# Optimization experiments

Hardware: AMD Instinct MI355X
Metric: run time of the kernel (lower is better)

## Reference

```python
import jax, jax.numpy as jnp
import numpy as np

N = 500000   # total objects across all segments
B = 8192     # number of segments (batch)
OBJ = 64     # object_size
H = 128      # hidden_size
CTX = 256    # context_size


def setup_inputs() -> dict:
    key = jax.random.key(0)
    ks = jax.random.split(key, 9)
    s = 0.05
    x = jax.random.normal(ks[0], (N, OBJ), jnp.float32)
    context = jax.random.normal(ks[1], (B, CTX), jnp.float32)
    # sorted segment ids, every segment nonempty (ragged lengths collapse to ~N/B each)
    segment_ids = (jnp.arange(N, dtype=jnp.int32) * B) // N
    W0 = jax.random.normal(ks[2], (OBJ, H), jnp.float32) * s
    b0 = jnp.zeros((H,), jnp.float32)
    W1 = jax.random.normal(ks[3], (H, H), jnp.float32) * s
    b1 = jnp.zeros((H,), jnp.float32)
    Wkv = jax.random.normal(ks[4], (H, 2 * H), jnp.float32) * s
    bkv = jnp.zeros((2 * H,), jnp.float32)
    Wq = jax.random.normal(ks[5], (CTX, H), jnp.float32) * s
    bq = jnp.zeros((H,), jnp.float32)
    gain = jnp.full((1, 1), -0.5 * np.log(H), jnp.float32)
    return dict(x=x, context=context, segment_ids=segment_ids,
                W0=W0, b0=b0, W1=W1, b1=b1, Wkv=Wkv, bkv=bkv,
                Wq=Wq, bq=bq, gain=gain)


def reference(x, context, segment_ids, W0, b0, W1, b1, Wkv, bkv, Wq, bq, gain):
    h = jax.nn.relu(x @ W0 + b0)          # [N, H]
    h = jax.nn.relu(h @ W1 + b1)          # [N, H]
    kv = h @ Wkv + bkv                    # [N, 2H]
    hsz = Wkv.shape[1] // 2
    key_, value = kv[:, :hsz], kv[:, hsz:]
    q = context @ Wq + bq                 # [B, H]
    qg = q[segment_ids]                   # gather == repeat_interleave
    logits = jnp.exp(gain)[0, 0] * jnp.sum(key_ * qg, axis=1)  # [N]
    # per-segment stable softmax
    m = jax.ops.segment_max(logits, segment_ids, num_segments=B)
    z = jnp.exp(logits - m[segment_ids])
    denom = jax.ops.segment_sum(z, segment_ids, num_segments=B)
    w = z / denom[segment_ids]            # [N]
    # per-segment softmax-weighted sum of values -> [B, H]
    embedding = jax.ops.segment_sum(w[:, None] * value, segment_ids, num_segments=B)
    return embedding, w[:, None]
```

## Files before the change

### kernel.cpp

```cpp
#include <hip/hip_runtime.h>
#include <math.h>

#define NN   500000
#define BB   8192
#define OBJ  64
#define HH   128
#define CTXD 256

typedef __attribute__((ext_vector_type(8))) short short8;
typedef __attribute__((ext_vector_type(4))) float f32x4;

#define W0HI  0
#define W0LO  8192
#define W1HI  16384
#define W1LO  32768
#define QG_OFF  98304
#define PG_OFF  4292608
#define CQ_OFF  8486912
#define WS_NEED 8519680

__device__ __forceinline__ unsigned short f2bf(float f) {
    unsigned int u = __float_as_uint(f);
    u += 0x7FFFu + ((u >> 16) & 1u);
    return (unsigned short)(u >> 16);
}
__device__ __forceinline__ float bf2f(unsigned short h) {
    return __uint_as_float(((unsigned int)h) << 16);
}
__device__ __forceinline__ void split2(float v, unsigned short& hi, unsigned short& lo) {
    unsigned int u = __float_as_uint(v);
    hi = (unsigned short)(u >> 16);
    lo = f2bf(v - bf2f(hi));
}

__global__ void prep_frags(const float* __restrict__ W0,
                           const float* __restrict__ W1,
                           unsigned short* __restrict__ wsb)
{
    const int t = blockIdx.x * 256 + threadIdx.x;
    if (t >= 48 * 64) return;
    const int f = t >> 6, lane = t & 63;
    const float* W; int KS, bhi, blo, fl;
    if (f < 16) { W = W0; KS = 2; bhi = W0HI; blo = W0LO; fl = f; }
    else        { W = W1; KS = 4; bhi = W1HI; blo = W1LO; fl = f - 16; }
    const int nt = fl / KS, ks = fl - nt * KS;
    const int n  = nt * 16 + (lane & 15);
    const int k0 = ks * 32 + (lane >> 4) * 8;
    short8 h8, l8;
    #pragma unroll
    for (int j = 0; j < 8; ++j) {
        float v = W[(size_t)(k0 + j) * HH + n];
        unsigned short h, l; split2(v, h, l);
        h8[j] = (short)h; l8[j] = (short)l;
    }
    const int off = fl * 512 + lane * 8;
    *(short8*)(wsb + bhi + off) = h8;
    *(short8*)(wsb + blo + off) = l8;
}

__global__ void q_gemm(const float* __restrict__ context,
                       const float* __restrict__ Wq,
                       const float* __restrict__ bq,
                       float* __restrict__ qg)
{
    __shared__ float ctxs[16 * CTXD];
    const int tid = threadIdx.x;
    const int seg0 = blockIdx.x * 16;
    {
        const float4* cg = (const float4*)(context + (size_t)seg0 * CTXD);
        float4* cs = (float4*)ctxs;
        for (int i = tid; i < 16 * CTXD / 4; i += 128) cs[i] = cg[i];
    }
    __syncthreads();
    float acc[16];
    const float bqv = bq[tid];
    #pragma unroll
    for (int s = 0; s < 16; ++s) acc[s] = bqv;
    #pragma unroll 4
    for (int k = 0; k < CTXD; ++k) {
        const float wv = Wq[(size_t)k * HH + tid];
        #pragma unroll
        for (int s = 0; s < 16; ++s) acc[s] = fmaf(ctxs[s * CTXD + k], wv, acc[s]);
    }
    #pragma unroll
    for (int s = 0; s < 16; ++s) qg[(size_t)(seg0 + s) * HH + tid] = acc[s];
}

__global__ void p_gemm(const float* __restrict__ qg,
                       const float* __restrict__ Wkv,
                       const float* __restrict__ bkv,
                       float* __restrict__ pg, float* __restrict__ cq)
{
    __shared__ float qs[16 * HH];
    const int tid = threadIdx.x;
    const int seg0 = blockIdx.x * 16;
    {
        const float4* sg = (const float4*)(qg + (size_t)seg0 * HH);
        float4* ss = (float4*)qs;
        for (int i = tid; i < 16 * HH / 4; i += 128) ss[i] = sg[i];
    }
    __syncthreads();
    float acc[16];
    #pragma unroll
    for (int s = 0; s < 16; ++s) acc[s] = 0.f;
    for (int c = 0; c < HH; ++c) {
        const float wv = Wkv[(size_t)tid * 2 * HH + c];
        #pragma unroll
        for (int s = 0; s < 16; ++s) acc[s] = fmaf(qs[s * HH + c], wv, acc[s]);
    }
    #pragma unroll
    for (int s = 0; s < 16; ++s) pg[(size_t)(seg0 + s) * HH + tid] = acc[s];
    if (tid < 16) {
        float a = 0.f;
        for (int c = 0; c < HH; ++c) a = fmaf(bkv[c], qs[tid * HH + c], a);
        cq[seg0 + tid] = a;
    }
}

#define BS 40

__launch_bounds__(64, 1)
__global__ void seg_wave(const float* __restrict__ x,
                         const float* __restrict__ context,
                         const float* __restrict__ Wq,   const float* __restrict__ bq,
                         const float* __restrict__ Wkv,  const float* __restrict__ bkv,
                         const float* __restrict__ b0,
                         const float* __restrict__ b1,
                         const float* __restrict__ gain,
                         const unsigned short* __restrict__ wsb,
                         const float* __restrict__ pg,
                         const float* __restrict__ cq,
                         float* __restrict__ out_emb, float* __restrict__ out_w)
{
    __shared__ unsigned short smem[2 * 64 * BS];
    const int lane = threadIdx.x;
    const int seg  = blockIdx.x;
    const int nl = lane & 15, q = lane >> 4;

    unsigned short* bufh = smem;
    unsigned short* bufl = smem + 64 * BS;
    float* fscr = (float*)smem;

    const int start = (int)(((long long)seg * NN + BB - 1) / BB);
    const int end   = (int)(((long long)(seg + 1) * NN + BB - 1) / BB);
    const int count = end - start;

    float b0v[8], b1v[8];
    #pragma unroll
    for (int nt = 0; nt < 8; ++nt) { b0v[nt] = b0[nt * 16 + nl]; b1v[nt] = b1[nt * 16 + nl]; }

    short8 axh[2][4], axl[2][4];
    #pragma unroll
    for (int ks = 0; ks < 2; ++ks) {
        #pragma unroll
        for (int mt = 0; mt < 4; ++mt) {
            int row = start + mt * 16 + nl;
            if (row > NN - 1) row = NN - 1;
            const float* xp = x + (size_t)row * OBJ + ks * 32 + q * 8;
            const float4 a0 = *(const float4*)xp;
            const float4 a1 = *(const float4*)(xp + 4);
            const float vv[8] = {a0.x, a0.y, a0.z, a0.w, a1.x, a1.y, a1.z, a1.w};
            #pragma unroll
            for (int j = 0; j < 8; ++j) {
                unsigned short h, l; split2(vv[j], h, l);
                axh[ks][mt][j] = (short)h; axl[ks][mt][j] = (short)l;
            }
        }
    }

    f32x4 acc2[8][4];
    #pragma unroll
    for (int nt = 0; nt < 8; ++nt)
        #pragma unroll
        for (int mt = 0; mt < 4; ++mt) acc2[nt][mt] = {0.f, 0.f, 0.f, 0.f};

    #pragma unroll
    for (int j = 0; j < 4; ++j) {
        f32x4 a1acc[2][4];
        #pragma unroll
        for (int t = 0; t < 2; ++t)
            #pragma unroll
            for (int mt = 0; mt < 4; ++mt) a1acc[t][mt] = {0.f, 0.f, 0.f, 0.f};
        #pragma unroll
        for (int ks = 0; ks < 2; ++ks) {
            #pragma unroll
            for (int t = 0; t < 2; ++t) {
                const int fb = ((2 * j + t) * 2 + ks) * 512 + lane * 8;
                const short8 bh = *(const short8*)(wsb + W0HI + fb);
                const short8 bl = *(const short8*)(wsb + W0LO + fb);
                #pragma unroll
                for (int mt = 0; mt < 4; ++mt) {
                    a1acc[t][mt] = __builtin_amdgcn_mfma_f32_16x16x32_bf16(axh[ks][mt], bh, a1acc[t][mt], 0, 0, 0);
                    a1acc[t][mt] = __builtin_amdgcn_mfma_f32_16x16x32_bf16(axh[ks][mt], bl, a1acc[t][mt], 0, 0, 0);
                    a1acc[t][mt] = __builtin_amdgcn_mfma_f32_16x16x32_bf16(axl[ks][mt], bh, a1acc[t][mt], 0, 0, 0);
                }
            }
        }
        #pragma unroll
        for (int t = 0; t < 2; ++t) {
            const float bb = b0v[2 * j + t];
            #pragma unroll
            for (int mt = 0; mt < 4; ++mt) {
                #pragma unroll
                for (int r = 0; r < 4; ++r) {
                    const int R = mt * 16 + q * 4 + r;
                    float hv = fmaxf(a1acc[t][mt][r] + bb, 0.f);
                    unsigned short h, l; split2(hv, h, l);
                    bufh[R * BS + t * 16 + nl] = h;
                    bufl[R * BS + t * 16 + nl] = l;
                }
            }
        }
        __asm__ volatile("s_waitcnt lgkmcnt(0)" ::: "memory");
        short8 ah[4], al[4];
        #pragma unroll
        for (int mt = 0; mt < 4; ++mt) {
            ah[mt] = *(const short8*)(bufh + (mt * 16 + nl) * BS + q * 8);
            al[mt] = *(const short8*)(bufl + (mt * 16 + nl) * BS + q * 8);
        }
        #pragma unroll
        for (int nt = 0; nt < 8; ++nt) {
            const int fb = (nt * 4 + j) * 512 + lane * 8;
            const short8 bh = *(const short8*)(wsb + W1HI + fb);
            const short8 bl = *(const short8*)(wsb + W1LO + fb);
            #pragma unroll
            for (int mt = 0; mt < 4; ++mt) {
                acc2[nt][mt] = __builtin_amdgcn_mfma_f32_16x16x32_bf16(ah[mt], bh, acc2[nt][mt], 0, 0, 0);
                acc2[nt][mt] = __builtin_amdgcn_mfma_f32_16x16x32_bf16(ah[mt], bl, acc2[nt][mt], 0, 0, 0);
                acc2[nt][mt] = __builtin_amdgcn_mfma_f32_16x16x32_bf16(al[mt], bh, acc2[nt][mt], 0, 0, 0);
            }
        }
        __asm__ volatile("s_waitcnt lgkmcnt(0)" ::: "memory");
    }

    #pragma unroll
    for (int nt = 0; nt < 8; ++nt)
        #pragma unroll
        for (int mt = 0; mt < 4; ++mt)
            #pragma unroll
            for (int r = 0; r < 4; ++r)
                acc2[nt][mt][r] = fmaxf(acc2[nt][mt][r] + b1v[nt], 0.f);

    float pv[8], cqv;
    if (pg) {
        #pragma unroll
        for (int nt = 0; nt < 8; ++nt) pv[nt] = pg[(size_t)seg * HH + nt * 16 + nl];
        cqv = cq[seg];
    } else {
        const int c0 = lane, c1 = lane + 64;
        float qa = bq[c0], qb = bq[c1];
        for (int k = 0; k < CTXD; ++k) {
            const float ck = context[(size_t)seg * CTXD + k];
            qa = fmaf(ck, Wq[(size_t)k * HH + c0], qa);
            qb = fmaf(ck, Wq[(size_t)k * HH + c1], qb);
        }
        fscr[c0] = qa; fscr[c1] = qb;
        __asm__ volatile("s_waitcnt lgkmcnt(0)" ::: "memory");
        cqv = 0.f;
        for (int c = 0; c < HH; ++c) cqv = fmaf(bkv[c], fscr[c], cqv);
        #pragma unroll
        for (int nt = 0; nt < 8; ++nt) {
            const int k = nt * 16 + nl;
            float s = 0.f;
            for (int c = 0; c < HH; ++c) s = fmaf(Wkv[(size_t)k * 2 * HH + c], fscr[c], s);
            pv[nt] = s;
        }
        __asm__ volatile("s_waitcnt lgkmcnt(0)" ::: "memory");
    }

    const float eg = expf(gain[0]);
    float lp[4][4];
    #pragma unroll
    for (int mt = 0; mt < 4; ++mt) {
        #pragma unroll
        for (int r = 0; r < 4; ++r) {
            float s = 0.f;
            #pragma unroll
            for (int nt = 0; nt < 8; ++nt) s = fmaf(acc2[nt][mt][r], pv[nt], s);
            #pragma unroll
            for (int off = 1; off <= 8; off <<= 1) s += __shfl_xor(s, off, 64);
            const int row = mt * 16 + q * 4 + r;
            lp[mt][r] = (row < count) ? eg * (s + cqv) : -INFINITY;
        }
    }

    float m = lp[0][0];
    #pragma unroll
    for (int mt = 0; mt < 4; ++mt)
        #pragma unroll
        for (int r = 0; r < 4; ++r) m = fmaxf(m, lp[mt][r]);
    m = fmaxf(m, __shfl_xor(m, 16, 64));
    m = fmaxf(m, __shfl_xor(m, 32, 64));
    float wv[4][4], Z = 0.f;
    #pragma unroll
    for (int mt = 0; mt < 4; ++mt)
        #pragma unroll
        for (int r = 0; r < 4; ++r) { wv[mt][r] = expf(lp[mt][r] - m); Z += wv[mt][r]; }
    Z += __shfl_xor(Z, 16, 64);
    Z += __shfl_xor(Z, 32, 64);
    const float rZ = 1.f / Z;
    #pragma unroll
    for (int mt = 0; mt < 4; ++mt)
        #pragma unroll
        for (int r = 0; r < 4; ++r) wv[mt][r] *= rZ;
    if (nl == 0) {
        #pragma unroll
        for (int mt = 0; mt < 4; ++mt)
            #pragma unroll
            for (int r = 0; r < 4; ++r) {
                const int row = mt * 16 + q * 4 + r;
                if (row < count) out_w[start + row] = wv[mt][r];
            }
    }

    float un[8];
    #pragma unroll
    for (int nt = 0; nt < 8; ++nt) {
        float s = 0.f;
        #pragma unroll
        for (int mt = 0; mt < 4; ++mt)
            #pragma unroll
            for (int r = 0; r < 4; ++r) s = fmaf(wv[mt][r], acc2[nt][mt][r], s);
        s += __shfl_xor(s, 16, 64);
        s += __shfl_xor(s, 32, 64);
        un[nt] = s;
    }
    __asm__ volatile("s_waitcnt lgkmcnt(0)" ::: "memory");
    if (q == 0) {
        #pragma unroll
        for (int nt = 0; nt < 8; ++nt) fscr[nt * 16 + nl] = un[nt];
    }
    __asm__ volatile("s_waitcnt lgkmcnt(0)" ::: "memory");

    {
        const int c0 = lane, c1 = lane + 64;
        float e0 = bkv[HH + c0], e1 = bkv[HH + c1];
        #pragma unroll 4
        for (int k = 0; k < HH; ++k) {
            const float uk = fscr[k];
            e0 = fmaf(uk, Wkv[(size_t)k * 2 * HH + HH + c0], e0);
            e1 = fmaf(uk, Wkv[(size_t)k * 2 * HH + HH + c1], e1);
        }
        out_emb[(size_t)seg * HH + c0] = e0;
        out_emb[(size_t)seg * HH + c1] = e1;
    }
}

extern "C" void kernel_launch(void* const* d_in, const int* in_sizes, int n_in,
                              void* d_out, int out_size, void* d_ws, size_t ws_size,
                              hipStream_t stream)
{
    (void)in_sizes; (void)n_in; (void)out_size;
    const float* x    = (const float*)d_in[0];
    const float* ctx  = (const float*)d_in[1];
    const float* W0   = (const float*)d_in[3];
    const float* b0   = (const float*)d_in[4];
    const float* W1   = (const float*)d_in[5];
    const float* b1   = (const float*)d_in[6];
    const float* Wkv  = (const float*)d_in[7];
    const float* bkv  = (const float*)d_in[8];
    const float* Wq   = (const float*)d_in[9];
    const float* bq   = (const float*)d_in[10];
    const float* gain = (const float*)d_in[11];

    float* out_emb = (float*)d_out;
    float* out_w   = (float*)d_out + (size_t)BB * HH;

    unsigned short* wsb = (unsigned short*)d_ws;
    const bool big_ws = (ws_size >= (size_t)WS_NEED);
    float* qg = big_ws ? (float*)((char*)d_ws + QG_OFF) : nullptr;
    float* pg = big_ws ? (float*)((char*)d_ws + PG_OFF) : nullptr;
    float* cq = big_ws ? (float*)((char*)d_ws + CQ_OFF) : nullptr;

    hipLaunchKernelGGL(prep_frags, dim3(12), dim3(256), 0, stream, W0, W1, wsb);
    if (big_ws) {
        hipLaunchKernelGGL(q_gemm, dim3(BB / 16), dim3(128), 0, stream, ctx, Wq, bq, qg);
        hipLaunchKernelGGL(p_gemm, dim3(BB / 16), dim3(128), 0, stream, qg, Wkv, bkv, pg, cq);
    }
    hipLaunchKernelGGL(seg_wave, dim3(BB), dim3(64), 0, stream,
                       x, ctx, Wq, bq, Wkv, bkv, b0, b1, gain, wsb, pg, cq,
                       out_emb, out_w);
}
```

Baseline: 413.6 us.

## Stage x tiles in swizzled LDS, split embedding GEMM out, transpose Wkv for p_gemm

The x tile is now converted to bf16 hi/lo pairs into XOR-swizzled shared memory instead of being held as register fragments. Hidden activations also move to a swizzled layout, and launch bounds rise to two waves per SIMD to improve occupancy. The final value projection leaves the per-segment wave: unnormalised sums go to a workspace buffer and a separate batched emb_gemm kernel applies Wkv. p_gemm reads a pre-transposed Wkv for coalesced loads. In exchange, the change adds two kernel launches and more global traffic, and it depends on the workspace overlap of qg and ug being safe.

```diff
diff --git a/kernel.cpp b/kernel.cpp
--- a/kernel.cpp
+++ b/kernel.cpp
@@ -14,10 +14,12 @@
 #define W0LO  8192
 #define W1HI  16384
 #define W1LO  32768
-#define QG_OFF  98304
-#define PG_OFF  4292608
-#define CQ_OFF  8486912
-#define WS_NEED 8519680
+#define WKT_OFF 98304
+#define QG_OFF  163840
+#define UG_OFF  163840
+#define PG_OFF  4358144
+#define CQ_OFF  8552448
+#define WS_NEED 8585216
 
 __device__ __forceinline__ unsigned short f2bf(float f) {
     unsigned int u = __float_as_uint(f);
@@ -58,6 +60,16 @@
     *(short8*)(wsb + blo + off) = l8;
 }
 
+__global__ void wk_t(const float* __restrict__ Wkv, float* __restrict__ wkt)
+{
+    __shared__ float tile[16][17];
+    const int tx = threadIdx.x, ty = threadIdx.y;
+    const int k0 = blockIdx.x * 16, c0 = blockIdx.y * 16;
+    tile[ty][tx] = Wkv[(size_t)(k0 + ty) * 2 * HH + c0 + tx];
+    __syncthreads();
+    wkt[(size_t)(c0 + ty) * HH + k0 + tx] = tile[tx][ty];
+}
+
 __global__ void q_gemm(const float* __restrict__ context,
                        const float* __restrict__ Wq,
                        const float* __restrict__ bq,
@@ -87,7 +99,7 @@
 }
 
 __global__ void p_gemm(const float* __restrict__ qg,
-                       const float* __restrict__ Wkv,
+                       const float* __restrict__ wkt,
                        const float* __restrict__ bkv,
                        float* __restrict__ pg, float* __restrict__ cq)
 {
@@ -103,8 +115,9 @@
     float acc[16];
     #pragma unroll
     for (int s = 0; s < 16; ++s) acc[s] = 0.f;
+    #pragma unroll 4
     for (int c = 0; c < HH; ++c) {
-        const float wv = Wkv[(size_t)tid * 2 * HH + c];
+        const float wv = wkt[(size_t)c * HH + tid];
         #pragma unroll
         for (int s = 0; s < 16; ++s) acc[s] = fmaf(qs[s * HH + c], wv, acc[s]);
     }
@@ -117,9 +130,35 @@
     }
 }
 
-#define BS 40
-
-__launch_bounds__(64, 1)
+__global__ void emb_gemm(const float* __restrict__ ug,
+                         const float* __restrict__ Wkv,
+                         const float* __restrict__ bkv,
+                         float* __restrict__ out_emb)
+{
+    __shared__ float us[16 * HH];
+    const int tid = threadIdx.x;
+    const int seg0 = blockIdx.x * 16;
+    {
+        const float4* sg = (const float4*)(ug + (size_t)seg0 * HH);
+        float4* ss = (float4*)us;
+        for (int i = tid; i < 16 * HH / 4; i += 128) ss[i] = sg[i];
+    }
+    __syncthreads();
+    float acc[16];
+    const float bv = bkv[HH + tid];
+    #pragma unroll
+    for (int s = 0; s < 16; ++s) acc[s] = bv;
+    #pragma unroll 4
+    for (int k = 0; k < HH; ++k) {
+        const float wv = Wkv[(size_t)k * 2 * HH + HH + tid];
+        #pragma unroll
+        for (int s = 0; s < 16; ++s) acc[s] = fmaf(us[s * HH + k], wv, acc[s]);
+    }
+    #pragma unroll
+    for (int s = 0; s < 16; ++s) out_emb[(size_t)(seg0 + s) * HH + tid] = acc[s];
+}
+
+__launch_bounds__(64, 2)
 __global__ void seg_wave(const float* __restrict__ x,
                          const float* __restrict__ context,
                          const float* __restrict__ Wq,   const float* __restrict__ bq,
@@ -130,43 +169,55 @@
                          const unsigned short* __restrict__ wsb,
                          const float* __restrict__ pg,
                          const float* __restrict__ cq,
+                         float* __restrict__ ug,
                          float* __restrict__ out_emb, float* __restrict__ out_w)
 {
-    __shared__ unsigned short smem[2 * 64 * BS];
+    __shared__ unsigned short smem[12288];
+    unsigned short* xh = smem;
+    unsigned short* xl = smem + 4096;
+    unsigned short* hh = smem + 8192;
+    unsigned short* hl = smem + 10240;
+    float* fscr = (float*)smem;
+
     const int lane = threadIdx.x;
     const int seg  = blockIdx.x;
     const int nl = lane & 15, q = lane >> 4;
 
-    unsigned short* bufh = smem;
-    unsigned short* bufl = smem + 64 * BS;
-    float* fscr = (float*)smem;
-
     const int start = (int)(((long long)seg * NN + BB - 1) / BB);
     const int end   = (int)(((long long)(seg + 1) * NN + BB - 1) / BB);
     const int count = end - start;
 
+    float pv[8], cqv = 0.f;
+    if (pg) {
+        #pragma unroll
+        for (int nt = 0; nt < 8; ++nt) pv[nt] = pg[(size_t)seg * HH + nt * 16 + nl];
+        cqv = cq[seg];
+    }
     float b0v[8], b1v[8];
     #pragma unroll
     for (int nt = 0; nt < 8; ++nt) { b0v[nt] = b0[nt * 16 + nl]; b1v[nt] = b1[nt * 16 + nl]; }
 
-    short8 axh[2][4], axl[2][4];
-    #pragma unroll
-    for (int ks = 0; ks < 2; ++ks) {
-        #pragma unroll
-        for (int mt = 0; mt < 4; ++mt) {
-            int row = start + mt * 16 + nl;
-            if (row > NN - 1) row = NN - 1;
-            const float* xp = x + (size_t)row * OBJ + ks * 32 + q * 8;
-            const float4 a0 = *(const float4*)xp;
-            const float4 a1 = *(const float4*)(xp + 4);
-            const float vv[8] = {a0.x, a0.y, a0.z, a0.w, a1.x, a1.y, a1.z, a1.w};
-            #pragma unroll
-            for (int j = 0; j < 8; ++j) {
-                unsigned short h, l; split2(vv[j], h, l);
-                axh[ks][mt][j] = (short)h; axl[ks][mt][j] = (short)l;
-            }
-        }
-    }
+    #pragma unroll
+    for (int it = 0; it < 8; ++it) {
+        const int i = it * 64 + lane;
+        const int row = i >> 3, g = i & 7;
+        int grow = start + row;
+        if (grow > NN - 1) grow = NN - 1;
+        const float* xp = x + (size_t)grow * OBJ + g * 8;
+        const float4 a0 = *(const float4*)xp;
+        const float4 a1 = *(const float4*)(xp + 4);
+        const float vv[8] = {a0.x, a0.y, a0.z, a0.w, a1.x, a1.y, a1.z, a1.w};
+        short8 h8, l8;
+        #pragma unroll
+        for (int j = 0; j < 8; ++j) {
+            unsigned short h, l; split2(vv[j], h, l);
+            h8[j] = (short)h; l8[j] = (short)l;
+        }
+        const int off = row * 64 + ((g ^ (row & 7)) << 3);
+        *(short8*)(xh + off) = h8;
+        *(short8*)(xl + off) = l8;
+    }
+    __asm__ volatile("s_waitcnt lgkmcnt(0)" ::: "memory");
 
     f32x4 acc2[8][4];
     #pragma unroll
@@ -183,31 +234,42 @@
             for (int mt = 0; mt < 4; ++mt) a1acc[t][mt] = {0.f, 0.f, 0.f, 0.f};
         #pragma unroll
         for (int ks = 0; ks < 2; ++ks) {
+            short8 bh[2], bl[2];
             #pragma unroll
             for (int t = 0; t < 2; ++t) {
                 const int fb = ((2 * j + t) * 2 + ks) * 512 + lane * 8;
-                const short8 bh = *(const short8*)(wsb + W0HI + fb);
-                const short8 bl = *(const short8*)(wsb + W0LO + fb);
+                bh[t] = *(const short8*)(wsb + W0HI + fb);
+                bl[t] = *(const short8*)(wsb + W0LO + fb);
+            }
+            const int grp = ks * 4 + q;
+            #pragma unroll
+            for (int mt = 0; mt < 4; ++mt) {
+                const int row = mt * 16 + nl;
+                const int off = row * 64 + ((grp ^ (row & 7)) << 3);
+                const short8 ahi = *(const short8*)(xh + off);
+                const short8 alo = *(const short8*)(xl + off);
                 #pragma unroll
-                for (int mt = 0; mt < 4; ++mt) {
-                    a1acc[t][mt] = __builtin_amdgcn_mfma_f32_16x16x32_bf16(axh[ks][mt], bh, a1acc[t][mt], 0, 0, 0);
-                    a1acc[t][mt] = __builtin_amdgcn_mfma_f32_16x16x32_bf16(axh[ks][mt], bl, a1acc[t][mt], 0, 0, 0);
-                    a1acc[t][mt] = __builtin_amdgcn_mfma_f32_16x16x32_bf16(axl[ks][mt], bh, a1acc[t][mt], 0, 0, 0);
+                for (int t = 0; t < 2; ++t) {
+                    a1acc[t][mt] = __builtin_amdgcn_mfma_f32_16x16x32_bf16(ahi, bh[t], a1acc[t][mt], 0, 0, 0);
+                    a1acc[t][mt] = __builtin_amdgcn_mfma_f32_16x16x32_bf16(ahi, bl[t], a1acc[t][mt], 0, 0, 0);
+                    a1acc[t][mt] = __builtin_amdgcn_mfma_f32_16x16x32_bf16(alo, bh[t], a1acc[t][mt], 0, 0, 0);
                 }
             }
         }
         #pragma unroll
         for (int t = 0; t < 2; ++t) {
             const float bb = b0v[2 * j + t];
+            const int cg = t * 2 + (nl >> 3);
             #pragma unroll
             for (int mt = 0; mt < 4; ++mt) {
                 #pragma unroll
                 for (int r = 0; r < 4; ++r) {
                     const int R = mt * 16 + q * 4 + r;
+                    const int off = R * 32 + (((cg ^ (R & 3)) & 3) << 3) + (nl & 7);
                     float hv = fmaxf(a1acc[t][mt][r] + bb, 0.f);
                     unsigned short h, l; split2(hv, h, l);
-                    bufh[R * BS + t * 16 + nl] = h;
-                    bufl[R * BS + t * 16 + nl] = l;
+                    hh[off] = h;
+                    hl[off] = l;
                 }
             }
         }
@@ -215,8 +277,10 @@
         short8 ah[4], al[4];
         #pragma unroll
         for (int mt = 0; mt < 4; ++mt) {
-            ah[mt] = *(const short8*)(bufh + (mt * 16 + nl) * BS + q * 8);
-            al[mt] = *(const short8*)(bufl + (mt * 16 + nl) * BS + q * 8);
+            const int m = mt * 16 + nl;
+            const int off = m * 32 + (((q ^ (m & 3)) & 3) << 3);
+            ah[mt] = *(const short8*)(hh + off);
+            al[mt] = *(const short8*)(hl + off);
         }
         #pragma unroll
         for (int nt = 0; nt < 8; ++nt) {
@@ -241,12 +305,7 @@
             for (int r = 0; r < 4; ++r)
                 acc2[nt][mt][r] = fmaxf(acc2[nt][mt][r] + b1v[nt], 0.f);
 
-    float pv[8], cqv;
-    if (pg) {
-        #pragma unroll
-        for (int nt = 0; nt < 8; ++nt) pv[nt] = pg[(size_t)seg * HH + nt * 16 + nl];
-        cqv = cq[seg];
-    } else {
+    if (!pg) {
         const int c0 = lane, c1 = lane + 64;
         float qa = bq[c0], qb = bq[c1];
         for (int k = 0; k < CTXD; ++k) {
@@ -325,14 +384,18 @@
         s += __shfl_xor(s, 32, 64);
         un[nt] = s;
     }
-    __asm__ volatile("s_waitcnt lgkmcnt(0)" ::: "memory");
-    if (q == 0) {
-        #pragma unroll
-        for (int nt = 0; nt < 8; ++nt) fscr[nt * 16 + nl] = un[nt];
-    }
-    __asm__ volatile("s_waitcnt lgkmcnt(0)" ::: "memory");
-
-    {
+
+    if (ug) {
+        if (q == 0) {
+            #pragma unroll
+            for (int nt = 0; nt < 8; ++nt) ug[(size_t)seg * HH + nt * 16 + nl] = un[nt];
+        }
+    } else {
+        if (q == 0) {
+            #pragma unroll
+            for (int nt = 0; nt < 8; ++nt) fscr[nt * 16 + nl] = un[nt];
+        }
+        __asm__ volatile("s_waitcnt lgkmcnt(0)" ::: "memory");
         const int c0 = lane, c1 = lane + 64;
         float e0 = bkv[HH + c0], e1 = bkv[HH + c1];
         #pragma unroll 4
@@ -368,16 +431,22 @@
 
     unsigned short* wsb = (unsigned short*)d_ws;
     const bool big_ws = (ws_size >= (size_t)WS_NEED);
-    float* qg = big_ws ? (float*)((char*)d_ws + QG_OFF) : nullptr;
-    float* pg = big_ws ? (float*)((char*)d_ws + PG_OFF) : nullptr;
-    float* cq = big_ws ? (float*)((char*)d_ws + CQ_OFF) : nullptr;
+    float* wkt = big_ws ? (float*)((char*)d_ws + WKT_OFF) : nullptr;
+    float* qg  = big_ws ? (float*)((char*)d_ws + QG_OFF)  : nullptr;
+    float* ugp = big_ws ? (float*)((char*)d_ws + UG_OFF)  : nullptr;
+    float* pg  = big_ws ? (float*)((char*)d_ws + PG_OFF)  : nullptr;
+    float* cq  = big_ws ? (float*)((char*)d_ws + CQ_OFF)  : nullptr;
 
     hipLaunchKernelGGL(prep_frags, dim3(12), dim3(256), 0, stream, W0, W1, wsb);
     if (big_ws) {
+        hipLaunchKernelGGL(wk_t, dim3(8, 8), dim3(16, 16), 0, stream, Wkv, wkt);
         hipLaunchKernelGGL(q_gemm, dim3(BB / 16), dim3(128), 0, stream, ctx, Wq, bq, qg);
-        hipLaunchKernelGGL(p_gemm, dim3(BB / 16), dim3(128), 0, stream, qg, Wkv, bkv, pg, cq);
+        hipLaunchKernelGGL(p_gemm, dim3(BB / 16), dim3(128), 0, stream, qg, wkt, bkv, pg, cq);
     }
     hipLaunchKernelGGL(seg_wave, dim3(BB), dim3(64), 0, stream,
-                       x, ctx, Wq, bq, Wkv, bkv, b0, b1, gain, wsb, pg, cq,
+                       x, ctx, Wq, bq, Wkv, bkv, b0, b1, gain, wsb, pg, cq, ugp,
                        out_emb, out_w);
-}
+    if (big_ws)
+        hipLaunchKernelGGL(emb_gemm, dim3(BB / 16), dim3(128), 0, stream,
+                           ugp, Wkv, bkv, out_emb);
+}
```

Measured after the change: 467.3 us. 1.13x slower.
